# Performance work log

Hardware: AMD Instinct MI355X
Metric: run time of the kernel (lower is better)

## Reference

```python
import jax, jax.numpy as jnp
import numpy as np

NODES_PER_GRAPH = 21
NUM_GRAPHS = 50000
N = NODES_PER_GRAPH * NUM_GRAPHS  # 1,050,000 nodes
NUM_FEATURES = 3
NUM_CLASSES = 29
H1, H2 = 64, 128
BN_EPS = 1e-5

_HAND = np.array([(0, 1), (1, 2), (2, 3), (3, 4), (0, 5), (5, 6), (6, 7), (7, 8),
                  (0, 9), (9, 10), (10, 11), (11, 12), (0, 13), (13, 14), (14, 15),
                  (15, 16), (0, 17), (17, 18), (18, 19), (19, 20)], dtype=np.int64).T  # [2,20]


def setup_inputs() -> dict:
    key = jax.random.key(0)
    ks = jax.random.split(key, 16)
    # Tile hand skeleton across NUM_GRAPHS disjoint graphs with node offsets.
    offsets = (np.arange(NUM_GRAPHS, dtype=np.int64) * NODES_PER_GRAPH)  # [G]
    ei = (_HAND[:, None, :] + offsets[None, :, None]).reshape(2, -1)      # [2, G*20]
    edge_index = jnp.asarray(ei)
    batch = jnp.asarray(np.repeat(np.arange(NUM_GRAPHS, dtype=np.int64), NODES_PER_GRAPH))

    x = jax.random.normal(ks[0], (N, NUM_FEATURES), dtype=jnp.float32)

    def lin(k, fi, fo):
        kw, kb = jax.random.split(k)
        s = 1.0 / np.sqrt(fi)
        return (jax.random.uniform(kw, (fi, fo), jnp.float32, -s, s),
                jax.random.uniform(kb, (fo,), jnp.float32, -s, s))

    W1, b1 = lin(ks[1], NUM_FEATURES, H1)
    W2, b2 = lin(ks[2], H1, H2)
    W3, b3 = lin(ks[3], H2, NUM_CLASSES)

    def bn(k, d):
        k1, k2, k3, k4 = jax.random.split(k, 4)
        return (1.0 + 0.1 * jax.random.normal(k1, (d,), jnp.float32),   # gamma
                0.1 * jax.random.normal(k2, (d,), jnp.float32),          # beta
                0.01 * jax.random.normal(k3, (d,), jnp.float32),         # running_mean
                jax.random.uniform(k4, (d,), jnp.float32, 0.5, 1.5))     # running_var

    g1, be1, m1, v1 = bn(ks[4], H1)
    g2, be2, m2, v2 = bn(ks[5], H2)

    return {"x": x, "W1": W1, "b1": b1, "g1": g1, "be1": be1, "m1": m1, "v1": v1,
            "W2": W2, "b2": b2, "g2": g2, "be2": be2, "m2": m2, "v2": v2,
            "W3": W3, "b3": b3, "edge_index": edge_index, "batch": batch}


def gcn_conv(x, W, b, src, dst):
    """PyG GCNConv: linear, add self-loops, sym-normalized scatter-add, bias."""
    h = x @ W                                              # [N, Fout]
    deg = jnp.zeros((N,), x.dtype).at[dst].add(1.0) + 1.0  # in-degree incl. self-loop
    dinv = deg ** -0.5
    msg = h[src] * (dinv[src] * dinv[dst])[:, None]        # edge-wise gather + normalize
    out = jnp.zeros_like(h).at[dst].add(msg)               # scatter-add aggregation
    out = out + h * (dinv * dinv)[:, None]                 # self-loop contribution
    return out + b


def bn_eval(x, gamma, beta, mean, var):
    return (x - mean) * (gamma * jax.lax.rsqrt(var + BN_EPS)) + beta


def reference(x, W1, b1, g1, be1, m1, v1, W2, b2, g2, be2, m2, v2, W3, b3,
              edge_index, batch):
    src, dst = edge_index[0], edge_index[1]
    h = jax.nn.relu(bn_eval(gcn_conv(x, W1, b1, src, dst), g1, be1, m1, v1))
    # dropout is identity in eval mode
    h = jax.nn.relu(bn_eval(gcn_conv(h, W2, b2, src, dst), g2, be2, m2, v2))
    h = gcn_conv(h, W3, b3, src, dst)                      # [N, C]
    summed = jax.ops.segment_sum(h, batch, num_segments=NUM_GRAPHS)
    counts = jax.ops.segment_sum(jnp.ones((N,), h.dtype), batch, num_segments=NUM_GRAPHS)
    pooled = summed / counts[:, None]                      # global mean pool [G, C]
    return jax.nn.log_softmax(pooled, axis=1)
```

## Files before the change

### kernel.cpp

```cpp
#include <hip/hip_runtime.h>
#include <math.h>


#define G_TOTAL 50000
#define NPG 21
#define GPB 6
#define NCHUNK ((G_TOTAL + GPB - 1) / GPB)
#define NCLS 29
#define BN_EPS 1e-5f
#define INV_SQRT2 0.70710678118654752440f
#define ROOT_COLSUM 4.53553390593273762f

#define WS_W1B  0
#define WS_B2   256
#define WS_B3   384
#define WS_W3T  416
#define WS_BF   4128
#define WS_TOTAL (WS_BF + 4096)

typedef short s16x8 __attribute__((ext_vector_type(8)));
typedef float f32x4 __attribute__((ext_vector_type(4)));

__device__ __forceinline__ unsigned f2bf_rne(float f) {
    unsigned u = __float_as_uint(f);
    return (u + 0x7FFFu + ((u >> 16) & 1u)) >> 16;
}

__global__ void prep_kernel(const float* __restrict__ W1, const float* __restrict__ b1,
                            const float* __restrict__ g1, const float* __restrict__ be1,
                            const float* __restrict__ m1, const float* __restrict__ v1,
                            const float* __restrict__ W2, const float* __restrict__ b2,
                            const float* __restrict__ g2, const float* __restrict__ be2,
                            const float* __restrict__ m2, const float* __restrict__ v2,
                            const float* __restrict__ W3, const float* __restrict__ b3,
                            float* __restrict__ ws) {
    int t = blockIdx.x * blockDim.x + threadIdx.x;
    if (t < 256) {
        int k = t >> 2, comp = t & 3;
        float s = g1[k] * rsqrtf(v1[k] + BN_EPS);
        float v;
        if (comp < 3) v = W1[comp * 64 + k] * s;
        else          v = (b1[k] - m1[k]) * s + be1[k];
        ws[WS_W1B + t] = v;
    } else if (t < 384) {
        int j = t - 256;
        float s = g2[j] * rsqrtf(v2[j] + BN_EPS);
        ws[WS_B2 + j] = (b2[j] - m2[j]) * s + be2[j];
    } else if (t < 416) {
        int j = t - 384;
        ws[WS_B3 + j] = (j < NCLS) ? b3[j] : 0.f;
    } else if (t < WS_BF) {
        int i = t - WS_W3T;
        if (i < 3712) {
            int c = i >> 7, k = i & 127;
            ws[WS_W3T + i] = W3[k * NCLS + c];
        }
    } else if (t < WS_TOTAL) {
        int i = t - WS_BF;
        int d  = i & 3;
        int l  = (i >> 2) & 63;
        int ss = (i >> 8) & 1;
        int n  = i >> 9;
        int kg = l >> 4, r = l & 15;
        int c = 16 * n + r;
        float sc = g2[c] * rsqrtf(v2[c] + BN_EPS);
        int k0 = 32 * ss + 8 * kg + 2 * d;
        unsigned h0 = f2bf_rne(W2[k0 * 128 + c] * sc);
        unsigned h1 = f2bf_rne(W2[(k0 + 1) * 128 + c] * sc);
        ((unsigned*)ws)[WS_BF + i] = (h1 << 16) | h0;
    }
}

__global__ __launch_bounds__(256, 7)
void gcn_main(const float* __restrict__ x, const float* __restrict__ ws,
              float* __restrict__ out) {
    __shared__ __align__(16) float sFrag[4096];
    __shared__ __align__(16) float4 sW1B[64];
    __shared__ float sb2[128];
    __shared__ __align__(8) float2 sLUT[128];
    __shared__ __align__(16) float sP[GPB * 128];

    const int tid = threadIdx.x;
    const int g0 = blockIdx.x * GPB;
    const int nv = min(GPB, G_TOTAL - g0);
    const int Mrows = nv * NPG;

    if (tid < 64) sW1B[tid] = ((const float4*)ws)[tid];
    else if (tid < 192) sb2[tid - 64] = ws[WS_B2 + (tid - 64)];
    if (tid < 128) {
        const int r = tid;
        const int lg2 = (r * 3121) >> 16;
        const int j = r - NPG * lg2;
        float w = (j == 0) ? (ROOT_COLSUM / 21.f)
                           : (((j & 3) == 0) ? (0.5f / 21.f) : (1.f / 21.f));
        if (r >= Mrows) w = 0.f;
        sLUT[r] = make_float2(w, (float)lg2);
    }
    {
        const int n2 = (Mrows * 3) >> 1;
        const float2* xg2 = (const float2*)(x + (long long)g0 * 63);
        if (tid < n2) ((float2*)sP)[tid] = xg2[tid];
    }
    __syncthreads();

    const int node = tid >> 1;
    const int s = tid & 1;
    const int k0 = s * 32;
    const int lg = (node * 3121) >> 16;
    const int j21 = node - NPG * lg;
    const int dist = (j21 == 0) ? 0 : (((j21 & 3) == 1) ? j21 : 1);
    const float cw = ((j21 & 3) == 1) ? INV_SQRT2 : 0.5f;
    char* const fragB = (char*)sFrag + ((node >> 4) * 2 + s) * 1024 + (node & 15) * 16;
    float z[32];
    {
        const float* xs = (const float*)sP + node * 3;
        const float s0 = xs[0], s1 = xs[1], s2 = xs[2];
        const float* xq = xs - dist * 3;
        const float ax0 = fmaf(cw, xq[0], 0.5f * s0);
        const float ax1 = fmaf(cw, xq[1], 0.5f * s1);
        const float ax2 = fmaf(cw, xq[2], 0.5f * s2);
        #pragma unroll
        for (int kk = 0; kk < 32; ++kk) {
            const float4 wv = sW1B[k0 + kk];
            float t = fmaf(ax0, wv.x, wv.w);
            t = fmaf(ax1, wv.y, t);
            t = fmaf(ax2, wv.z, t);
            z[kk] = fmaxf(t, 0.f);
        }
        unsigned dw[16];
        #pragma unroll
        for (int p = 0; p < 16; ++p)
            dw[p] = __builtin_amdgcn_perm(__float_as_uint(z[2*p+1]),
                                          __float_as_uint(z[2*p]), 0x07060302u);
        #pragma unroll
        for (int g = 0; g < 4; ++g)
            *(uint4*)(fragB + g * 256) =
                make_uint4(dw[4*g], dw[4*g+1], dw[4*g+2], dw[4*g+3]);
    }
    __syncthreads();

    if (dist != 0) {
        const int prow = node - dist;
        const char* pfrag = (const char*)sFrag
                          + ((prow >> 4) * 2 + s) * 1024 + (prow & 15) * 16;
        #pragma unroll
        for (int g = 0; g < 4; ++g) {
            const uint4 pd = *(const uint4*)(pfrag + g * 256);
            const unsigned d4[4] = {pd.x, pd.y, pd.z, pd.w};
            #pragma unroll
            for (int d = 0; d < 4; ++d) {
                const float plo = __uint_as_float(d4[d] << 16);
                const float phi = __uint_as_float(d4[d] & 0xFFFF0000u);
                z[8*g + 2*d]     = fmaf(cw, plo, 0.5f * z[8*g + 2*d]);
                z[8*g + 2*d + 1] = fmaf(cw, phi, 0.5f * z[8*g + 2*d + 1]);
            }
        }
    }
    __syncthreads();

    {
        unsigned dw[16];
        #pragma unroll
        for (int p = 0; p < 16; ++p)
            dw[p] = __builtin_amdgcn_perm(__float_as_uint(z[2*p+1]),
                                          __float_as_uint(z[2*p]), 0x07060302u);
        #pragma unroll
        for (int g = 0; g < 4; ++g)
            *(uint4*)(fragB + g * 256) =
                make_uint4(dw[4*g], dw[4*g+1], dw[4*g+2], dw[4*g+3]);
    }
    __syncthreads();

    {
        const int w = tid >> 6;
        const int lane = tid & 63;
        const int r = lane & 15;
        const int g4 = lane >> 4;
        const uint4* wsB = (const uint4*)((const unsigned*)ws + WS_BF);
        uint4 B00 = wsB[((2*w+0)*2 + 0)*64 + lane];
        uint4 B01 = wsB[((2*w+0)*2 + 1)*64 + lane];
        uint4 B10 = wsB[((2*w+1)*2 + 0)*64 + lane];
        uint4 B11 = wsB[((2*w+1)*2 + 1)*64 + lane];
        const float b2c0 = sb2[32*w + r];
        const float b2c1 = sb2[32*w + 16 + r];
        const float2* lutp = &sLUT[4 * g4];
        const char* fragA = (const char*)sFrag + lane * 16;

        float pg[GPB][2];
        #pragma unroll
        for (int g = 0; g < GPB; ++g) { pg[g][0] = 0.f; pg[g][1] = 0.f; }

        #pragma unroll
        for (int m = 0; m < 8; ++m) {
            const s16x8 A0 = *(const s16x8*)(fragA + (2*m + 0) * 1024);
            const s16x8 A1 = *(const s16x8*)(fragA + (2*m + 1) * 1024);
            f32x4 acc0 = {0.f, 0.f, 0.f, 0.f};
            f32x4 acc1 = {0.f, 0.f, 0.f, 0.f};
            acc0 = __builtin_amdgcn_mfma_f32_16x16x32_bf16(A0, *(const s16x8*)&B00, acc0, 0, 0, 0);
            acc0 = __builtin_amdgcn_mfma_f32_16x16x32_bf16(A1, *(const s16x8*)&B01, acc0, 0, 0, 0);
            acc1 = __builtin_amdgcn_mfma_f32_16x16x32_bf16(A0, *(const s16x8*)&B10, acc1, 0, 0, 0);
            acc1 = __builtin_amdgcn_mfma_f32_16x16x32_bf16(A1, *(const s16x8*)&B11, acc1, 0, 0, 0);

            #pragma unroll
            for (int i = 0; i < 4; ++i) {
                const float2 wg = lutp[16*m + i];
                const float t0 = fmaxf(acc0[i] + b2c0, 0.f) * wg.x;
                const float t1 = fmaxf(acc1[i] + b2c1, 0.f) * wg.x;
                const int lo = (16*m + i) / 21;
                const int hiRaw = (16*m + i + 12) / 21;
                const int hi = (hiRaw > 5) ? 5 : hiRaw;
                if (lo == hiRaw) {
                    pg[lo][0] += t0; pg[lo][1] += t1;
                } else {
                    const bool cA = (wg.y == (float)lo);
                    const float s0 = cA ? t0 : 0.f;
                    const float s1 = cA ? t1 : 0.f;
                    pg[lo][0] += s0; pg[hi][0] += t0 - s0;
                    pg[lo][1] += s1; pg[hi][1] += t1 - s1;
                }
            }
        }
        #pragma unroll
        for (int g = 0; g < GPB; ++g) {
            #pragma unroll
            for (int c = 0; c < 2; ++c) {
                float v = pg[g][c];
                v += __shfl_xor(v, 16);
                v += __shfl_xor(v, 32);
                pg[g][c] = v;
            }
        }
        if (lane < 16) {
            #pragma unroll
            for (int g = 0; g < GPB; ++g) {
                sP[g * 128 + 32*w + r]      = pg[g][0];
                sP[g * 128 + 32*w + 16 + r] = pg[g][1];
            }
        }
    }
    __syncthreads();

    float* sLg = sFrag;
    if (tid < GPB * NCLS) {
        const int g = (tid * 2260) >> 16;
        const int c = tid - g * NCLS;
        const float4* w3 = (const float4*)(ws + WS_W3T + c * 128);
        const float4* pp = (const float4*)&sP[g * 128];
        float acc3 = ws[WS_B3 + c];
        #pragma unroll
        for (int k = 0; k < 32; ++k) {
            const float4 wv = w3[k];
            const float4 pv = pp[k];
            acc3 = fmaf(pv.x, wv.x, acc3);
            acc3 = fmaf(pv.y, wv.y, acc3);
            acc3 = fmaf(pv.z, wv.z, acc3);
            acc3 = fmaf(pv.w, wv.w, acc3);
        }
        sLg[tid] = acc3;
    }
    __syncthreads();

    if (tid < 192) {
        const int g = tid >> 5, c = tid & 31;
        const bool act = (c < NCLS) && (g < nv);
        float v = act ? sLg[g * NCLS + c] : -1e30f;
        float m = v;
        m = fmaxf(m, __shfl_xor(m, 1));
        m = fmaxf(m, __shfl_xor(m, 2));
        m = fmaxf(m, __shfl_xor(m, 4));
        m = fmaxf(m, __shfl_xor(m, 8));
        m = fmaxf(m, __shfl_xor(m, 16));
        float e = act ? expf(v - m) : 0.f;
        float ss = e;
        ss += __shfl_xor(ss, 1);
        ss += __shfl_xor(ss, 2);
        ss += __shfl_xor(ss, 4);
        ss += __shfl_xor(ss, 8);
        ss += __shfl_xor(ss, 16);
        if (act)
            out[(long long)g0 * NCLS + g * NCLS + c] = v - m - logf(ss);
    }
}

extern "C" void kernel_launch(void* const* d_in, const int* in_sizes, int n_in,
                              void* d_out, int out_size, void* d_ws, size_t ws_size,
                              hipStream_t stream) {
    const float* x   = (const float*)d_in[0];
    const float* W1  = (const float*)d_in[1];
    const float* b1  = (const float*)d_in[2];
    const float* g1  = (const float*)d_in[3];
    const float* be1 = (const float*)d_in[4];
    const float* m1  = (const float*)d_in[5];
    const float* v1  = (const float*)d_in[6];
    const float* W2  = (const float*)d_in[7];
    const float* b2  = (const float*)d_in[8];
    const float* g2  = (const float*)d_in[9];
    const float* be2 = (const float*)d_in[10];
    const float* m2  = (const float*)d_in[11];
    const float* v2  = (const float*)d_in[12];
    const float* W3  = (const float*)d_in[13];
    const float* b3  = (const float*)d_in[14];
    float* out = (float*)d_out;
    float* ws  = (float*)d_ws;

    prep_kernel<<<(WS_TOTAL + 255) / 256, 256, 0, stream>>>(
        W1, b1, g1, be1, m1, v1, W2, b2, g2, be2, m2, v2, W3, b3, ws);

    gcn_main<<<NCHUNK, 256, 0, stream>>>(x, ws, out);
}
```

Before: 200.9 us.

## Reorganize tile layout by node position across 4 graphs, recompute parent aggregation

Switches from 6 graphs per block with linear row packing to 4 graphs per block with a position-major layout: MFMA rows hold the same hand-node index across the 4 graphs, so each lane accumulates one graph with compile-time pooling weights. This removes the LUT, the straddling-graph select logic and the cross-lane shuffle reduction. Layer-1 neighbor aggregation is now done by recomputing the parent's relu output from raw inputs instead of an extra LDS round trip with two barriers. It also uses a padded tile stride, a higher occupancy bound and fast exp/log intrinsics. The trade-off is more blocks, duplicated layer-1 arithmetic, and 168 of 256 threads active in phase one.

```diff
diff --git a/kernel.cpp b/kernel.cpp
--- a/kernel.cpp
+++ b/kernel.cpp
@@ -3,13 +3,12 @@
 
 
 #define G_TOTAL 50000
-#define NPG 21
-#define GPB 6
-#define NCHUNK ((G_TOTAL + GPB - 1) / GPB)
+#define GPB 4
+#define NBLK (G_TOTAL / GPB)
 #define NCLS 29
 #define BN_EPS 1e-5f
 #define INV_SQRT2 0.70710678118654752440f
-#define ROOT_COLSUM 4.53553390593273762f
+#define ROOT_W 0.21597780504441608f
 
 #define WS_W1B  0
 #define WS_B2   256
@@ -17,6 +16,8 @@
 #define WS_W3T  416
 #define WS_BF   4128
 #define WS_TOTAL (WS_BF + 4096)
+
+#define TSTRIDE 1056
 
 typedef short s16x8 __attribute__((ext_vector_type(8)));
 typedef float f32x4 __attribute__((ext_vector_type(4)));
@@ -71,103 +72,69 @@
     }
 }
 
-__global__ __launch_bounds__(256, 7)
+__global__ __launch_bounds__(256, 8)
 void gcn_main(const float* __restrict__ x, const float* __restrict__ ws,
               float* __restrict__ out) {
-    __shared__ __align__(16) float sFrag[4096];
+    __shared__ __align__(16) char sFrag[12 * TSTRIDE];
     __shared__ __align__(16) float4 sW1B[64];
-    __shared__ float sb2[128];
-    __shared__ __align__(8) float2 sLUT[128];
-    __shared__ __align__(16) float sP[GPB * 128];
+    __shared__ __align__(16) float sPX[512];
 
     const int tid = threadIdx.x;
-    const int g0 = blockIdx.x * GPB;
-    const int nv = min(GPB, G_TOTAL - g0);
-    const int Mrows = nv * NPG;
+    const long long blk = blockIdx.x;
 
     if (tid < 64) sW1B[tid] = ((const float4*)ws)[tid];
-    else if (tid < 192) sb2[tid - 64] = ws[WS_B2 + (tid - 64)];
-    if (tid < 128) {
-        const int r = tid;
-        const int lg2 = (r * 3121) >> 16;
-        const int j = r - NPG * lg2;
-        float w = (j == 0) ? (ROOT_COLSUM / 21.f)
-                           : (((j & 3) == 0) ? (0.5f / 21.f) : (1.f / 21.f));
-        if (r >= Mrows) w = 0.f;
-        sLUT[r] = make_float2(w, (float)lg2);
-    }
-    {
-        const int n2 = (Mrows * 3) >> 1;
-        const float2* xg2 = (const float2*)(x + (long long)g0 * 63);
-        if (tid < n2) ((float2*)sP)[tid] = xg2[tid];
-    }
-    __syncthreads();
-
-    const int node = tid >> 1;
-    const int s = tid & 1;
-    const int k0 = s * 32;
-    const int lg = (node * 3121) >> 16;
-    const int j21 = node - NPG * lg;
-    const int dist = (j21 == 0) ? 0 : (((j21 & 3) == 1) ? j21 : 1);
-    const float cw = ((j21 & 3) == 1) ? INV_SQRT2 : 0.5f;
-    char* const fragB = (char*)sFrag + ((node >> 4) * 2 + s) * 1024 + (node & 15) * 16;
-    float z[32];
-    {
-        const float* xs = (const float*)sP + node * 3;
-        const float s0 = xs[0], s1 = xs[1], s2 = xs[2];
+    if (tid < 63) ((float4*)sPX)[tid] = ((const float4*)(x + blk * 252))[tid];
+    if (tid >= 64 && tid < 64 + 132)
+        *(float4*)(sFrag + 10 * TSTRIDE + (tid - 64) * 16) =
+            make_float4(0.f, 0.f, 0.f, 0.f);
+    __syncthreads();
+
+    if (tid < 168) {
+        const int node = tid >> 1;
+        const int s = tid & 1;
+        const int k0 = s * 32;
+        const int g4 = (node * 3121) >> 16;
+        const int p  = node - 21 * g4;
+        const int dist  = (p == 0) ? 0 : (((p & 3) == 1) ? p : 1);
+        const float cw  = ((p & 3) == 1) ? INV_SQRT2 : 0.5f;
+        const int jp = p - dist;
+        const int dist2 = (jp == 0) ? 0 : (((jp & 3) == 1) ? jp : 1);
+        const float cw2 = ((jp & 3) == 1) ? INV_SQRT2 : 0.5f;
+
+        const float* xs = (const float*)sPX + node * 3;
         const float* xq = xs - dist * 3;
-        const float ax0 = fmaf(cw, xq[0], 0.5f * s0);
-        const float ax1 = fmaf(cw, xq[1], 0.5f * s1);
-        const float ax2 = fmaf(cw, xq[2], 0.5f * s2);
+        const float* xg = xq - dist2 * 3;
+        const float ax0 = fmaf(cw,  xq[0], 0.5f * xs[0]);
+        const float ax1 = fmaf(cw,  xq[1], 0.5f * xs[1]);
+        const float ax2 = fmaf(cw,  xq[2], 0.5f * xs[2]);
+        const float bx0 = fmaf(cw2, xg[0], 0.5f * xq[0]);
+        const float bx1 = fmaf(cw2, xg[1], 0.5f * xq[1]);
+        const float bx2 = fmaf(cw2, xg[2], 0.5f * xq[2]);
+
+        float az[32];
         #pragma unroll
         for (int kk = 0; kk < 32; ++kk) {
             const float4 wv = sW1B[k0 + kk];
-            float t = fmaf(ax0, wv.x, wv.w);
-            t = fmaf(ax1, wv.y, t);
-            t = fmaf(ax2, wv.z, t);
-            z[kk] = fmaxf(t, 0.f);
+            float ts = fmaf(ax0, wv.x, wv.w);
+            ts = fmaf(ax1, wv.y, ts);
+            ts = fmaf(ax2, wv.z, ts);
+            ts = fmaxf(ts, 0.f);
+            float tp = fmaf(bx0, wv.x, wv.w);
+            tp = fmaf(bx1, wv.y, tp);
+            tp = fmaf(bx2, wv.z, tp);
+            tp = fmaxf(tp, 0.f);
+            az[kk] = fmaf(cw, tp, 0.5f * ts);
         }
         unsigned dw[16];
         #pragma unroll
-        for (int p = 0; p < 16; ++p)
-            dw[p] = __builtin_amdgcn_perm(__float_as_uint(z[2*p+1]),
-                                          __float_as_uint(z[2*p]), 0x07060302u);
-        #pragma unroll
-        for (int g = 0; g < 4; ++g)
-            *(uint4*)(fragB + g * 256) =
-                make_uint4(dw[4*g], dw[4*g+1], dw[4*g+2], dw[4*g+3]);
-    }
-    __syncthreads();
-
-    if (dist != 0) {
-        const int prow = node - dist;
-        const char* pfrag = (const char*)sFrag
-                          + ((prow >> 4) * 2 + s) * 1024 + (prow & 15) * 16;
-        #pragma unroll
-        for (int g = 0; g < 4; ++g) {
-            const uint4 pd = *(const uint4*)(pfrag + g * 256);
-            const unsigned d4[4] = {pd.x, pd.y, pd.z, pd.w};
-            #pragma unroll
-            for (int d = 0; d < 4; ++d) {
-                const float plo = __uint_as_float(d4[d] << 16);
-                const float phi = __uint_as_float(d4[d] & 0xFFFF0000u);
-                z[8*g + 2*d]     = fmaf(cw, plo, 0.5f * z[8*g + 2*d]);
-                z[8*g + 2*d + 1] = fmaf(cw, phi, 0.5f * z[8*g + 2*d + 1]);
-            }
-        }
-    }
-    __syncthreads();
-
-    {
-        unsigned dw[16];
-        #pragma unroll
-        for (int p = 0; p < 16; ++p)
-            dw[p] = __builtin_amdgcn_perm(__float_as_uint(z[2*p+1]),
-                                          __float_as_uint(z[2*p]), 0x07060302u);
-        #pragma unroll
-        for (int g = 0; g < 4; ++g)
-            *(uint4*)(fragB + g * 256) =
-                make_uint4(dw[4*g], dw[4*g+1], dw[4*g+2], dw[4*g+3]);
+        for (int q = 0; q < 16; ++q)
+            dw[q] = __builtin_amdgcn_perm(__float_as_uint(az[2*q+1]),
+                                          __float_as_uint(az[2*q]), 0x07060302u);
+        char* fragB = sFrag + ((p >> 2) * 2 + s) * TSTRIDE + (4 * g4 + (p & 3)) * 16;
+        #pragma unroll
+        for (int kg = 0; kg < 4; ++kg)
+            *(uint4*)(fragB + kg * 256) =
+                make_uint4(dw[4*kg], dw[4*kg+1], dw[4*kg+2], dw[4*kg+3]);
     }
     __syncthreads();
 
@@ -175,25 +142,21 @@
         const int w = tid >> 6;
         const int lane = tid & 63;
         const int r = lane & 15;
-        const int g4 = lane >> 4;
+        const int lg = lane >> 4;
         const uint4* wsB = (const uint4*)((const unsigned*)ws + WS_BF);
-        uint4 B00 = wsB[((2*w+0)*2 + 0)*64 + lane];
-        uint4 B01 = wsB[((2*w+0)*2 + 1)*64 + lane];
-        uint4 B10 = wsB[((2*w+1)*2 + 0)*64 + lane];
-        uint4 B11 = wsB[((2*w+1)*2 + 1)*64 + lane];
-        const float b2c0 = sb2[32*w + r];
-        const float b2c1 = sb2[32*w + 16 + r];
-        const float2* lutp = &sLUT[4 * g4];
-        const char* fragA = (const char*)sFrag + lane * 16;
-
-        float pg[GPB][2];
-        #pragma unroll
-        for (int g = 0; g < GPB; ++g) { pg[g][0] = 0.f; pg[g][1] = 0.f; }
-
-        #pragma unroll
-        for (int m = 0; m < 8; ++m) {
-            const s16x8 A0 = *(const s16x8*)(fragA + (2*m + 0) * 1024);
-            const s16x8 A1 = *(const s16x8*)(fragA + (2*m + 1) * 1024);
+        const uint4 B00 = wsB[((2*w+0)*2 + 0)*64 + lane];
+        const uint4 B01 = wsB[((2*w+0)*2 + 1)*64 + lane];
+        const uint4 B10 = wsB[((2*w+1)*2 + 0)*64 + lane];
+        const uint4 B11 = wsB[((2*w+1)*2 + 1)*64 + lane];
+        const float b2c0 = ws[WS_B2 + 32*w + r];
+        const float b2c1 = ws[WS_B2 + 32*w + 16 + r];
+        const char* fragA = sFrag + lane * 16;
+
+        float pg0 = 0.f, pg1 = 0.f;
+        #pragma unroll
+        for (int m = 0; m < 6; ++m) {
+            const s16x8 A0 = *(const s16x8*)(fragA + (2*m + 0) * TSTRIDE);
+            const s16x8 A1 = *(const s16x8*)(fragA + (2*m + 1) * TSTRIDE);
             f32x4 acc0 = {0.f, 0.f, 0.f, 0.f};
             f32x4 acc1 = {0.f, 0.f, 0.f, 0.f};
             acc0 = __builtin_amdgcn_mfma_f32_16x16x32_bf16(A0, *(const s16x8*)&B00, acc0, 0, 0, 0);
@@ -203,49 +166,26 @@
 
             #pragma unroll
             for (int i = 0; i < 4; ++i) {
-                const float2 wg = lutp[16*m + i];
-                const float t0 = fmaxf(acc0[i] + b2c0, 0.f) * wg.x;
-                const float t1 = fmaxf(acc1[i] + b2c1, 0.f) * wg.x;
-                const int lo = (16*m + i) / 21;
-                const int hiRaw = (16*m + i + 12) / 21;
-                const int hi = (hiRaw > 5) ? 5 : hiRaw;
-                if (lo == hiRaw) {
-                    pg[lo][0] += t0; pg[lo][1] += t1;
-                } else {
-                    const bool cA = (wg.y == (float)lo);
-                    const float s0 = cA ? t0 : 0.f;
-                    const float s1 = cA ? t1 : 0.f;
-                    pg[lo][0] += s0; pg[hi][0] += t0 - s0;
-                    pg[lo][1] += s1; pg[hi][1] += t1 - s1;
+                const int p = 4*m + i;
+                if (p < 21) {
+                    const float wgt = (p == 0) ? ROOT_W
+                                    : (((p & 3) == 0) ? (0.5f / 21.f) : (1.f / 21.f));
+                    pg0 = fmaf(wgt, fmaxf(acc0[i] + b2c0, 0.f), pg0);
+                    pg1 = fmaf(wgt, fmaxf(acc1[i] + b2c1, 0.f), pg1);
                 }
             }
         }
-        #pragma unroll
-        for (int g = 0; g < GPB; ++g) {
-            #pragma unroll
-            for (int c = 0; c < 2; ++c) {
-                float v = pg[g][c];
-                v += __shfl_xor(v, 16);
-                v += __shfl_xor(v, 32);
-                pg[g][c] = v;
-            }
-        }
-        if (lane < 16) {
-            #pragma unroll
-            for (int g = 0; g < GPB; ++g) {
-                sP[g * 128 + 32*w + r]      = pg[g][0];
-                sP[g * 128 + 32*w + 16 + r] = pg[g][1];
-            }
-        }
-    }
-    __syncthreads();
-
-    float* sLg = sFrag;
+        sPX[lg * 128 + 32*w + r]      = pg0;
+        sPX[lg * 128 + 32*w + 16 + r] = pg1;
+    }
+    __syncthreads();
+
+    float* sLg = (float*)sFrag;
     if (tid < GPB * NCLS) {
         const int g = (tid * 2260) >> 16;
         const int c = tid - g * NCLS;
         const float4* w3 = (const float4*)(ws + WS_W3T + c * 128);
-        const float4* pp = (const float4*)&sP[g * 128];
+        const float4* pp = (const float4*)&sPX[g * 128];
         float acc3 = ws[WS_B3 + c];
         #pragma unroll
         for (int k = 0; k < 32; ++k) {
@@ -260,9 +200,9 @@
     }
     __syncthreads();
 
-    if (tid < 192) {
+    if (tid < 128) {
         const int g = tid >> 5, c = tid & 31;
-        const bool act = (c < NCLS) && (g < nv);
+        const bool act = (c < NCLS);
         float v = act ? sLg[g * NCLS + c] : -1e30f;
         float m = v;
         m = fmaxf(m, __shfl_xor(m, 1));
@@ -270,7 +210,7 @@
         m = fmaxf(m, __shfl_xor(m, 4));
         m = fmaxf(m, __shfl_xor(m, 8));
         m = fmaxf(m, __shfl_xor(m, 16));
-        float e = act ? expf(v - m) : 0.f;
+        float e = act ? __expf(v - m) : 0.f;
         float ss = e;
         ss += __shfl_xor(ss, 1);
         ss += __shfl_xor(ss, 2);
@@ -278,7 +218,7 @@
         ss += __shfl_xor(ss, 8);
         ss += __shfl_xor(ss, 16);
         if (act)
-            out[(long long)g0 * NCLS + g * NCLS + c] = v - m - logf(ss);
+            out[blk * (GPB * NCLS) + g * NCLS + c] = v - m - __logf(ss);
     }
 }
 
@@ -306,5 +246,5 @@
     prep_kernel<<<(WS_TOTAL + 255) / 256, 256, 0, stream>>>(
         W1, b1, g1, be1, m1, v1, W2, b2, g2, be2, m2, v2, W3, b3, ws);
 
-    gcn_main<<<NCHUNK, 256, 0, stream>>>(x, ws, out);
-}
+    gcn_main<<<NBLK, 256, 0, stream>>>(x, ws, out);
+}
```

After: 196.0 us. 1.02x faster.
